# Kernel optimization log

Hardware: AMD Instinct MI355X
Metric: run time of the kernel (lower is better)

The kernel has to match this reference:

```python
import jax, jax.numpy as jnp
import numpy as np

B, N, D = 4, 4096, 1024       # batch, seq_len, model dim
H, DH = 16, 64                # heads, dim per head
W = 256                       # sliding window size (causal: keys in [i-W+1, i])


def setup_inputs() -> dict:
    key = jax.random.key(0)
    k1, k2, k3 = jax.random.split(key, 3)
    x = jax.random.normal(k1, (B, N, D), dtype=jnp.float32)
    w_qkv = jax.random.normal(k2, (D, 3 * H * DH), dtype=jnp.float32) * (D ** -0.5)
    w_out = jax.random.normal(k3, (H * DH, D), dtype=jnp.float32) * ((H * DH) ** -0.5)
    return {"x": x, "w_qkv": w_qkv, "w_out": w_out}


def _sliding_window_attn(q, k, v):
    """Causal sliding-window attention, banded (block-local) computation.

    q,k,v: [BH, N, DH]; query i attends keys j with i-W+1 <= j <= i.
    Identical math to masking a full NxN score matrix with -finfo.max then softmax.
    """
    BH, n, dh = q.shape
    nb = n // W  # N is a multiple of W
    qb = q.reshape(BH, nb, W, dh)
    pad = jnp.zeros((BH, W, dh), q.dtype)
    kp = jnp.concatenate([pad, k], axis=1).reshape(BH, nb + 1, W, dh)
    vp = jnp.concatenate([pad, v], axis=1).reshape(BH, nb + 1, W, dh)
    # each query block sees previous block + current block of keys -> 2W keys
    kw = jnp.concatenate([kp[:, :-1], kp[:, 1:]], axis=2)  # [BH, nb, 2W, dh]
    vw = jnp.concatenate([vp[:, :-1], vp[:, 1:]], axis=2)
    scores = jnp.einsum('bnqd,bnkd->bnqk', qb, kw)  # [BH, nb, W, 2W]
    blk = jnp.arange(nb)[:, None, None]
    ii = jnp.arange(W)[None, :, None]
    jj = jnp.arange(2 * W)[None, None, :]
    # absolute key index = blk*W + jj - W ; absolute query index = blk*W + ii
    mask = (jj - W <= ii) & (jj >= ii + 1) & (blk * W + jj - W >= 0)
    neg = -jnp.finfo(scores.dtype).max  # matches torch max_neg_value
    scores = jnp.where(mask[None], scores, neg)
    attn = jax.nn.softmax(scores, axis=-1)
    out = jnp.einsum('bnqk,bnkd->bnqd', attn, vw)
    return out.reshape(BH, n, dh)


def reference(x, w_qkv, w_out):
    b, n, d = x.shape
    qkv = x @ w_qkv                      # [b, n, 3*H*DH]
    q, k, v = jnp.split(qkv, 3, axis=-1)

    def to_heads(t):  # b n (h d) -> (b h) n d
        return t.reshape(b, n, H, DH).transpose(0, 2, 1, 3).reshape(b * H, n, DH)

    q, k, v = map(to_heads, (q, k, v))
    q = q * (DH ** -0.5)                 # default scale = dim_head**-0.5
    out = _sliding_window_attn(q, k, v)  # [(b h), n, DH]
    out = out.reshape(b, H, n, DH).transpose(0, 2, 1, 3).reshape(b, n, H * DH)
    return out @ w_out
```

## Files before the change

kernel.cpp:

```cpp
#include <hip/hip_runtime.h>

typedef __attribute__((ext_vector_type(8))) short short8;
typedef __attribute__((ext_vector_type(4))) float floatx4;

#define AS1(p) ((const __attribute__((address_space(1))) void*)(uintptr_t)(p))
#define AS3(p) ((__attribute__((address_space(3))) void*)(unsigned int)(uintptr_t)(p))

__device__ __forceinline__ unsigned short f2bf(float f) {
    union { float f; unsigned int u; } v; v.f = f;
    unsigned int u = v.u;
    unsigned int r = (u + 0x7FFFu + ((u >> 16) & 1u)) >> 16;
    return (unsigned short)r;
}

__device__ __forceinline__ int pk_bf16(float a, float b) {
#if __has_builtin(__builtin_amdgcn_cvt_pk_bf16_f32)
    auto r = __builtin_amdgcn_cvt_pk_bf16_f32(a, b);
    int out; __builtin_memcpy(&out, &r, sizeof(int)); return out;
#else
    return (int)f2bf(a) | ((int)f2bf(b) << 16);
#endif
}

__global__ __launch_bounds__(256) void cvt_x(const float* __restrict__ src,
                                             unsigned short* __restrict__ dst, int n4) {
    int i = blockIdx.x * blockDim.x + threadIdx.x;
    if (i < n4) {
        float4 v = ((const float4*)src)[i];
        int2 o = {pk_bf16(v.x, v.y), pk_bf16(v.z, v.w)};
        ((int2*)dst)[i] = o;
    }
}

__global__ __launch_bounds__(256) void transpose_bf16(const float* __restrict__ src,
                                                      unsigned short* __restrict__ dst,
                                                      int R, int C) {
    __shared__ float tile[32][33];
    int c0 = blockIdx.x * 32, r0 = blockIdx.y * 32;
    int tc = threadIdx.x & 31, tr = (threadIdx.x >> 5) * 4;
#pragma unroll
    for (int i = 0; i < 4; ++i)
        tile[tr + i][tc] = src[(size_t)(r0 + tr + i) * C + c0 + tc];
    __syncthreads();
#pragma unroll
    for (int i = 0; i < 4; ++i)
        dst[(size_t)(c0 + tr + i) * R + r0 + tc] = f2bf(tile[tc][tr + i]);
}

template <bool OUT_BF16>
__global__ __launch_bounds__(256, 2) void gemm_bt128(const unsigned short* __restrict__ A,
                                                     const unsigned short* __restrict__ Bt,
                                                     void* __restrict__ Cout,
                                                     int M, int N, int K, int nbx) {
    __shared__ unsigned short Asm[2][128 * 32];
    __shared__ unsigned short Bsm[2][256 * 32];

    const int tid = threadIdx.x;
    const int wn = tid >> 6, lane = tid & 63, quad = lane >> 4, l15 = lane & 15;

    const int nwg = (int)gridDim.x;
    const int q8 = nwg >> 3;
    const int wgid = (int)blockIdx.x;
    const int swz = (wgid & 7) * q8 + (wgid >> 3);
    const int bm = (swz / nbx) * 128;
    const int bn = (swz % nbx) * 256;

    floatx4 acc[8][4];
    const floatx4 z = {0.f, 0.f, 0.f, 0.f};
#pragma unroll
    for (int mi = 0; mi < 8; ++mi)
#pragma unroll
        for (int ni = 0; ni < 4; ++ni) acc[mi][ni] = z;

    const int dA0 = tid, dA1 = tid + 256;
    const int rA0 = dA0 >> 2, cA0 = ((dA0 & 3) ^ ((dA0 >> 3) & 3)) * 8;
    const int rA1 = dA1 >> 2, cA1 = ((dA1 & 3) ^ ((dA1 >> 3) & 3)) * 8;
    const unsigned short* Asrc0 = A + (size_t)(bm + rA0) * K + cA0;
    const unsigned short* Asrc1 = A + (size_t)(bm + rA1) * K + cA1;
    const unsigned short* Bsrc[4];
    int dB[4];
#pragma unroll
    for (int j = 0; j < 4; ++j) {
        dB[j] = tid + j * 256;
        const int r = dB[j] >> 2, c = ((dB[j] & 3) ^ ((dB[j] >> 3) & 3)) * 8;
        Bsrc[j] = Bt + (size_t)(bn + r) * K + c;
    }

    const int NT = K >> 5;

    auto stage = [&](int t) {
        const int s = t & 1, ko = t * 32;
        __builtin_amdgcn_global_load_lds(AS1(Asrc0 + ko), AS3(&Asm[s][dA0 * 8]), 16, 0, 0);
        __builtin_amdgcn_global_load_lds(AS1(Asrc1 + ko), AS3(&Asm[s][dA1 * 8]), 16, 0, 0);
#pragma unroll
        for (int j = 0; j < 4; ++j)
            __builtin_amdgcn_global_load_lds(AS1(Bsrc[j] + ko), AS3(&Bsm[s][dB[j] * 8]), 16, 0, 0);
    };

    const int qc = (quad ^ ((l15 >> 1) & 3)) * 8;
    const int brow = wn * 64 + l15;

    stage(0);
    asm volatile("s_waitcnt vmcnt(0)" ::: "memory");
    __builtin_amdgcn_s_barrier();

    for (int t = 0; t < NT; ++t) {
        const int s = t & 1;
        const unsigned short* Ap = Asm[s];
        const unsigned short* Bp = Bsm[s];
        if (t + 1 < NT) stage(t + 1);

        short8 b[4], a0[4], a1[4];
#pragma unroll
        for (int ni = 0; ni < 4; ++ni)
            b[ni] = *(const short8*)&Bp[(brow + ni * 16) * 32 + qc];
#pragma unroll
        for (int mi = 0; mi < 4; ++mi)
            a0[mi] = *(const short8*)&Ap[(mi * 16 + l15) * 32 + qc];
#pragma unroll
        for (int mi = 0; mi < 4; ++mi)
            a1[mi] = *(const short8*)&Ap[(64 + mi * 16 + l15) * 32 + qc];

        __builtin_amdgcn_s_setprio(1);
#pragma unroll
        for (int mi = 0; mi < 4; ++mi)
#pragma unroll
            for (int ni = 0; ni < 4; ++ni)
                acc[mi][ni] = __builtin_amdgcn_mfma_f32_16x16x32_bf16(b[ni], a0[mi], acc[mi][ni], 0, 0, 0);
#pragma unroll
        for (int mi = 0; mi < 4; ++mi)
#pragma unroll
            for (int ni = 0; ni < 4; ++ni)
                acc[4 + mi][ni] = __builtin_amdgcn_mfma_f32_16x16x32_bf16(b[ni], a1[mi], acc[4 + mi][ni], 0, 0, 0);
        __builtin_amdgcn_s_setprio(0);

        asm volatile("s_waitcnt vmcnt(0)" ::: "memory");
        __builtin_amdgcn_s_barrier();
    }

#pragma unroll
    for (int mi = 0; mi < 8; ++mi) {
        const size_t row = (size_t)(bm + mi * 16 + l15);
#pragma unroll
        for (int ni = 0; ni < 4; ++ni) {
            const size_t col = (size_t)(bn + wn * 64 + ni * 16 + quad * 4);
            if (OUT_BF16) {
                int2 val = {pk_bf16(acc[mi][ni][0], acc[mi][ni][1]),
                            pk_bf16(acc[mi][ni][2], acc[mi][ni][3])};
                *(int2*)((unsigned short*)Cout + row * N + col) = val;
            } else {
                *(float4*)((float*)Cout + row * N + col) = *(const float4*)&acc[mi][ni];
            }
        }
    }
}

__global__ __launch_bounds__(256, 3) void attn_swin(const unsigned short* __restrict__ qkv,
                                                    unsigned short* __restrict__ attn_out) {
    __shared__ unsigned short Klds[2][64 * 72];
    __shared__ unsigned short Vtl[2][64 * 72];

    const int blk = blockIdx.x, bh = blockIdx.y;
    const int b = bh >> 4, h = bh & 15;
    const int tid = threadIdx.x;
    const int wave = tid >> 6, lane = tid & 63, quad = lane >> 4, l15 = lane & 15;
    const int pair = wave >> 1;
    const int qoff = (wave & 1) * 32;
    const int qi_base = blk * 128 + wave * 32;
    const size_t seqbase = (size_t)b * 4096;

    short8 qf[2][2];
#pragma unroll
    for (int qt = 0; qt < 2; ++qt)
#pragma unroll
        for (int ks = 0; ks < 2; ++ks)
            qf[qt][ks] = *(const short8*)(qkv + (seqbase + qi_base + qt * 16 + l15) * 3072
                                          + h * 64 + ks * 32 + quad * 8);

    floatx4 o[2][4];
    const floatx4 z = {0.f, 0.f, 0.f, 0.f};
    float m_run[2], l_run[2];
#pragma unroll
    for (int qt = 0; qt < 2; ++qt) {
#pragma unroll
        for (int dt = 0; dt < 4; ++dt) o[qt][dt] = z;
        m_run[qt] = -1.0e30f; l_run[qt] = 0.f;
    }

    const int kwin0 = blk * 128 - 256;
    const int c0 = (blk >= 2) ? 0 : (4 - 2 * blk);
    const int cLo = pair, cHi = pair + 4;
    const int sk_key = tid >> 2, sk_g = (tid & 3) * 16;
    const int sv_key = tid & 63, sv_dg = (tid >> 6) * 16;
    const float SC = 0.18033688f;

    const int addrA = (((quad & 1) << 5) + l15) << 2;
    const int addrB = addrA + 64;
    const bool hiq = quad >= 2;

    int4 kvreg[4];
    auto load_kv = [&](int k0) {
        const int4* sk = (const int4*)(qkv + (seqbase + k0 + sk_key) * 3072 + 1024 + h * 64 + sk_g);
        kvreg[0] = sk[0]; kvreg[1] = sk[1];
        const int4* sv = (const int4*)(qkv + (seqbase + k0 + sv_key) * 3072 + 2048 + h * 64 + sv_dg);
        kvreg[2] = sv[0]; kvreg[3] = sv[1];
    };
    auto write_kv = [&](int buf) {
        *(int4*)&Klds[buf][sk_key * 72 + sk_g]     = kvreg[0];
        *(int4*)&Klds[buf][sk_key * 72 + sk_g + 8] = kvreg[1];
        union { unsigned short s[16]; int4 q[2]; } t;
        t.q[0] = kvreg[2]; t.q[1] = kvreg[3];
#pragma unroll
        for (int i = 0; i < 16; ++i) Vtl[buf][(sv_dg + i) * 72 + sv_key] = t.s[i];
    };

    load_kv(kwin0 + c0 * 64);
    write_kv(0);

    for (int c = c0; c < 6; ++c) {
        const int buf = (c - c0) & 1;
        __syncthreads();
        if (c < 5) load_kv(kwin0 + (c + 1) * 64);

        if (c >= cLo && c <= cHi) {
#pragma unroll
            for (int qt = 0; qt < 2; ++qt) {
                floatx4 sT[4];
#pragma unroll
                for (int ni = 0; ni < 4; ++ni) sT[ni] = z;
#pragma unroll
                for (int ks = 0; ks < 2; ++ks) {
#pragma unroll
                    for (int ni = 0; ni < 4; ++ni) {
                        short8 kf = *(const short8*)&Klds[buf][(ni * 16 + l15) * 72 + ks * 32 + quad * 8];
                        sT[ni] = __builtin_amdgcn_mfma_f32_16x16x32_bf16(kf, qf[qt][ks], sT[ni], 0, 0, 0);
                    }
                }

                short8 vf[4][2];
#pragma unroll
                for (int dt = 0; dt < 4; ++dt)
#pragma unroll
                    for (int ks = 0; ks < 2; ++ks)
                        vf[dt][ks] = *(const short8*)&Vtl[buf][(dt * 16 + l15) * 72 + ks * 32 + quad * 8];

                const int i64 = qoff + qt * 16 + l15;
                if (c == cLo) {
#pragma unroll
                    for (int ni = 0; ni < 4; ++ni) {
                        int jb = ni * 16 + quad * 4;
#pragma unroll
                        for (int r = 0; r < 4; ++r)
                            if (jb + r < i64 + 1) sT[ni][r] = -3.0e38f;
                    }
                } else if (c == cHi) {
#pragma unroll
                    for (int ni = 0; ni < 4; ++ni) {
                        int jb = ni * 16 + quad * 4;
#pragma unroll
                        for (int r = 0; r < 4; ++r)
                            if (jb + r > i64) sT[ni][r] = -3.0e38f;
                    }
                }

                float mx = -3.0e38f;
#pragma unroll
                for (int ni = 0; ni < 4; ++ni)
#pragma unroll
                    for (int r = 0; r < 4; ++r) mx = fmaxf(mx, sT[ni][r]);
                mx = fmaxf(mx, __shfl_xor(mx, 16));
                mx = fmaxf(mx, __shfl_xor(mx, 32));
                float mn = fmaxf(m_run[qt], mx * SC);
                float alpha = __builtin_amdgcn_exp2f(m_run[qt] - mn);
                m_run[qt] = mn;

                float ls = 0.f;
                int Pk[4][2];
#pragma unroll
                for (int ni = 0; ni < 4; ++ni) {
                    float p0 = __builtin_amdgcn_exp2f(fmaf(sT[ni][0], SC, -mn));
                    float p1 = __builtin_amdgcn_exp2f(fmaf(sT[ni][1], SC, -mn));
                    float p2 = __builtin_amdgcn_exp2f(fmaf(sT[ni][2], SC, -mn));
                    float p3 = __builtin_amdgcn_exp2f(fmaf(sT[ni][3], SC, -mn));
                    ls += (p0 + p1) + (p2 + p3);
                    Pk[ni][0] = pk_bf16(p0, p1);
                    Pk[ni][1] = pk_bf16(p2, p3);
                }
                ls += __shfl_xor(ls, 16);
                ls += __shfl_xor(ls, 32);
                l_run[qt] = l_run[qt] * alpha + ls;
#pragma unroll
                for (int dt = 0; dt < 4; ++dt)
#pragma unroll
                    for (int r = 0; r < 4; ++r) o[qt][dt][r] *= alpha;

#pragma unroll
                for (int ks = 0; ks < 2; ++ks) {
                    int a0 = __builtin_amdgcn_ds_bpermute(addrA, Pk[2 * ks][0]);
                    int b0 = __builtin_amdgcn_ds_bpermute(addrA, Pk[2 * ks + 1][0]);
                    int a1 = __builtin_amdgcn_ds_bpermute(addrA, Pk[2 * ks][1]);
                    int b1 = __builtin_amdgcn_ds_bpermute(addrA, Pk[2 * ks + 1][1]);
                    int a2 = __builtin_amdgcn_ds_bpermute(addrB, Pk[2 * ks][0]);
                    int b2 = __builtin_amdgcn_ds_bpermute(addrB, Pk[2 * ks + 1][0]);
                    int a3 = __builtin_amdgcn_ds_bpermute(addrB, Pk[2 * ks][1]);
                    int b3 = __builtin_amdgcn_ds_bpermute(addrB, Pk[2 * ks + 1][1]);
                    union { int i[4]; short8 v; } u;
                    u.i[0] = hiq ? b0 : a0;
                    u.i[1] = hiq ? b1 : a1;
                    u.i[2] = hiq ? b2 : a2;
                    u.i[3] = hiq ? b3 : a3;
#pragma unroll
                    for (int dt = 0; dt < 4; ++dt)
                        o[qt][dt] = __builtin_amdgcn_mfma_f32_16x16x32_bf16(vf[dt][ks], u.v, o[qt][dt], 0, 0, 0);
                }
            }
        }

        if (c < 5) write_kv(buf ^ 1);
    }

#pragma unroll
    for (int qt = 0; qt < 2; ++qt) {
        float rl = __builtin_amdgcn_rcpf(l_run[qt]);
        size_t rowb = (seqbase + qi_base + qt * 16 + l15) * 1024 + h * 64;
#pragma unroll
        for (int dt = 0; dt < 4; ++dt) {
            int2 val = {pk_bf16(o[qt][dt][0] * rl, o[qt][dt][1] * rl),
                        pk_bf16(o[qt][dt][2] * rl, o[qt][dt][3] * rl)};
            *(int2*)(attn_out + rowb + dt * 16 + quad * 4) = val;
        }
    }
}

extern "C" void kernel_launch(void* const* d_in, const int* in_sizes, int n_in,
                              void* d_out, int out_size, void* d_ws, size_t ws_size,
                              hipStream_t stream) {
    const float* x     = (const float*)d_in[0];
    const float* w_qkv = (const float*)d_in[1];
    const float* w_out = (const float*)d_in[2];
    float* out = (float*)d_out;

    unsigned short* xb    = (unsigned short*)d_ws;
    unsigned short* wqkvT = xb    + (size_t)16384 * 1024;
    unsigned short* woutT = wqkvT + (size_t)3072 * 1024;
    unsigned short* qkv   = woutT + (size_t)1024 * 1024;
    unsigned short* attn  = qkv   + (size_t)16384 * 3072;

    cvt_x<<<16384, 256, 0, stream>>>(x, xb, 4194304);
    transpose_bf16<<<dim3(96, 32), 256, 0, stream>>>(w_qkv, wqkvT, 1024, 3072);
    transpose_bf16<<<dim3(32, 32), 256, 0, stream>>>(w_out, woutT, 1024, 1024);
    gemm_bt128<true><<<1536, 256, 0, stream>>>(xb, wqkvT, qkv, 16384, 3072, 1024, 12);
    attn_swin<<<dim3(32, 64), 256, 0, stream>>>(qkv, attn);
    gemm_bt128<false><<<512, 256, 0, stream>>>(attn, woutT, out, 16384, 1024, 1024, 4);
}
```

Baseline: 354.9 us.

## Stage K tiles via direct global-to-LDS loads with XOR swizzle in attention

In the sliding-window attention kernel, K tiles now go straight from global memory into LDS through global_load_lds with an XOR-swizzled, unpadded layout, so they no longer pass through registers. V fragment loads move to just before the PV MFMAs, s_setprio brackets the MFMA blocks, and launch bounds rise to allow 4 blocks per CU. The goal is fewer registers, more occupancy and less LDS write traffic for K. The swizzle has to agree exactly with the read-side chunk index, and the async LDS writes rely on the existing barrier to be visible before use.

```diff
diff --git a/kernel.cpp b/kernel.cpp
--- a/kernel.cpp
+++ b/kernel.cpp
@@ -155,9 +155,9 @@
     }
 }
 
-__global__ __launch_bounds__(256, 3) void attn_swin(const unsigned short* __restrict__ qkv,
+__global__ __launch_bounds__(256, 4) void attn_swin(const unsigned short* __restrict__ qkv,
                                                     unsigned short* __restrict__ attn_out) {
-    __shared__ unsigned short Klds[2][64 * 72];
+    __shared__ unsigned short Klds[2][64 * 64];
     __shared__ unsigned short Vtl[2][64 * 72];
 
     const int blk = blockIdx.x, bh = blockIdx.y;
@@ -190,37 +190,48 @@
     const int kwin0 = blk * 128 - 256;
     const int c0 = (blk >= 2) ? 0 : (4 - 2 * blk);
     const int cLo = pair, cHi = pair + 4;
-    const int sk_key = tid >> 2, sk_g = (tid & 3) * 16;
     const int sv_key = tid & 63, sv_dg = (tid >> 6) * 16;
     const float SC = 0.18033688f;
+
+    const int kd0 = tid, kd1 = tid + 256;
+    const int kr0 = kd0 >> 3, kc0s = ((kd0 & 7) ^ ((kd0 >> 3) & 7)) * 8;
+    const int kr1 = kd1 >> 3, kc1s = ((kd1 & 7) ^ ((kd1 >> 3) & 7)) * 8;
+    const int kch[2] = {((0 + quad) ^ (l15 & 7)) * 8, ((4 + quad) ^ (l15 & 7)) * 8};
 
     const int addrA = (((quad & 1) << 5) + l15) << 2;
     const int addrB = addrA + 64;
     const bool hiq = quad >= 2;
 
-    int4 kvreg[4];
-    auto load_kv = [&](int k0) {
-        const int4* sk = (const int4*)(qkv + (seqbase + k0 + sk_key) * 3072 + 1024 + h * 64 + sk_g);
-        kvreg[0] = sk[0]; kvreg[1] = sk[1];
+    auto stage_k = [&](int k0, int buf) {
+        const unsigned short* s0 = qkv + (seqbase + k0 + kr0) * 3072 + 1024 + h * 64 + kc0s;
+        const unsigned short* s1 = qkv + (seqbase + k0 + kr1) * 3072 + 1024 + h * 64 + kc1s;
+        __builtin_amdgcn_global_load_lds(AS1(s0), AS3(&Klds[buf][kd0 * 8]), 16, 0, 0);
+        __builtin_amdgcn_global_load_lds(AS1(s1), AS3(&Klds[buf][kd1 * 8]), 16, 0, 0);
+    };
+
+    int4 vreg[2];
+    auto load_v = [&](int k0) {
         const int4* sv = (const int4*)(qkv + (seqbase + k0 + sv_key) * 3072 + 2048 + h * 64 + sv_dg);
-        kvreg[2] = sv[0]; kvreg[3] = sv[1];
+        vreg[0] = sv[0]; vreg[1] = sv[1];
     };
-    auto write_kv = [&](int buf) {
-        *(int4*)&Klds[buf][sk_key * 72 + sk_g]     = kvreg[0];
-        *(int4*)&Klds[buf][sk_key * 72 + sk_g + 8] = kvreg[1];
+    auto write_v = [&](int buf) {
         union { unsigned short s[16]; int4 q[2]; } t;
-        t.q[0] = kvreg[2]; t.q[1] = kvreg[3];
+        t.q[0] = vreg[0]; t.q[1] = vreg[1];
 #pragma unroll
         for (int i = 0; i < 16; ++i) Vtl[buf][(sv_dg + i) * 72 + sv_key] = t.s[i];
     };
 
-    load_kv(kwin0 + c0 * 64);
-    write_kv(0);
+    stage_k(kwin0 + c0 * 64, 0);
+    load_v(kwin0 + c0 * 64);
+    write_v(0);
 
     for (int c = c0; c < 6; ++c) {
         const int buf = (c - c0) & 1;
         __syncthreads();
-        if (c < 5) load_kv(kwin0 + (c + 1) * 64);
+        if (c < 5) {
+            stage_k(kwin0 + (c + 1) * 64, buf ^ 1);
+            load_v(kwin0 + (c + 1) * 64);
+        }
 
         if (c >= cLo && c <= cHi) {
 #pragma unroll
@@ -228,21 +239,16 @@
                 floatx4 sT[4];
 #pragma unroll
                 for (int ni = 0; ni < 4; ++ni) sT[ni] = z;
+                __builtin_amdgcn_s_setprio(1);
 #pragma unroll
                 for (int ks = 0; ks < 2; ++ks) {
 #pragma unroll
                     for (int ni = 0; ni < 4; ++ni) {
-                        short8 kf = *(const short8*)&Klds[buf][(ni * 16 + l15) * 72 + ks * 32 + quad * 8];
+                        short8 kf = *(const short8*)&Klds[buf][(ni * 16 + l15) * 64 + kch[ks]];
                         sT[ni] = __builtin_amdgcn_mfma_f32_16x16x32_bf16(kf, qf[qt][ks], sT[ni], 0, 0, 0);
                     }
                 }
-
-                short8 vf[4][2];
-#pragma unroll
-                for (int dt = 0; dt < 4; ++dt)
-#pragma unroll
-                    for (int ks = 0; ks < 2; ++ks)
-                        vf[dt][ks] = *(const short8*)&Vtl[buf][(dt * 16 + l15) * 72 + ks * 32 + quad * 8];
+                __builtin_amdgcn_s_setprio(0);
 
                 const int i64 = qoff + qt * 16 + l15;
                 if (c == cLo) {
@@ -293,6 +299,13 @@
                 for (int dt = 0; dt < 4; ++dt)
 #pragma unroll
                     for (int r = 0; r < 4; ++r) o[qt][dt][r] *= alpha;
+
+                short8 vf[4][2];
+#pragma unroll
+                for (int dt = 0; dt < 4; ++dt)
+#pragma unroll
+                    for (int ks = 0; ks < 2; ++ks)
+                        vf[dt][ks] = *(const short8*)&Vtl[buf][(dt * 16 + l15) * 72 + ks * 32 + quad * 8];
 
 #pragma unroll
                 for (int ks = 0; ks < 2; ++ks) {
@@ -309,14 +322,16 @@
                     u.i[1] = hiq ? b1 : a1;
                     u.i[2] = hiq ? b2 : a2;
                     u.i[3] = hiq ? b3 : a3;
+                    __builtin_amdgcn_s_setprio(1);
 #pragma unroll
                     for (int dt = 0; dt < 4; ++dt)
                         o[qt][dt] = __builtin_amdgcn_mfma_f32_16x16x32_bf16(vf[dt][ks], u.v, o[qt][dt], 0, 0, 0);
+                    __builtin_amdgcn_s_setprio(0);
                 }
             }
         }
 
-        if (c < 5) write_kv(buf ^ 1);
+        if (c < 5) write_v(buf ^ 1);
     }
 
 #pragma unroll
```

New measurement: 373.0 us. +5.1%, slower.
